# Performance work log

Measured on AMD Instinct MI355X. Metric: run time of the kernel, lower is better.

Reference implementation:

```python
import jax, jax.numpy as jnp
import numpy as np

_EPS = 1e-5
RC = 5.0   # cutoff radius
L = 20     # number of radial basis functions
N = 10000  # nodes
E = 100000 # edges
F = 128    # in_feats


def _ssp(x):
    # ShiftedSoftplus: softplus(x) - log(2)
    return jax.nn.softplus(x) - jnp.log(2.0)


def _rbf(r):
    # DimeNet radial basis: sqrt(2/rc) * sin(n*pi*r/rc) / r, n = 1..L.  r: [E,1] -> [E,L]
    n = jnp.arange(1, L + 1, dtype=r.dtype)
    return jnp.sqrt(2.0 / RC) * jnp.sin(n * jnp.pi * r / RC) / r


def _fc(u):
    # cosine cutoff applied elementwise: 0.5*(cos(pi*u/rc)+1) for u < rc else 0
    return jnp.where(u < RC, 0.5 * (jnp.cos(jnp.pi * u / RC) + 1.0), 0.0)


def setup_inputs() -> dict:
    key = jax.random.key(0)
    ks = jax.random.split(key, 12)

    def nrm(k, shape, scale=1.0):
        return jax.random.normal(k, shape, dtype=jnp.float32) * scale

    return {
        "x": nrm(ks[0], (N, 3)) * 3.0,           # atomic positions
        "v": nrm(ks[1], (N, F, 3)),               # vector node features
        "s": nrm(ks[2], (N, F)),                  # scalar node features
        "ms1_w": nrm(ks[3], (F, F), F ** -0.5),
        "ms1_b": jnp.zeros((F,), jnp.float32),
        "ms2_w": nrm(ks[4], (3 * F, F), F ** -0.5),
        "ms2_b": jnp.zeros((3 * F,), jnp.float32),
        "mv_w": nrm(ks[5], (3 * F, L), L ** -0.5),
        "mv_b": jnp.zeros((3 * F,), jnp.float32),
        "us1_w": nrm(ks[6], (F, F), F ** -0.5),
        "us1_b": jnp.zeros((F,), jnp.float32),
        "us2_w": nrm(ks[7], (3 * F, F), F ** -0.5),
        "us2_b": jnp.zeros((3 * F,), jnp.float32),
        "src": jax.random.randint(ks[8], (E,), 0, N, dtype=jnp.int32),
        "dst": jax.random.randint(ks[9], (E,), 0, N, dtype=jnp.int32),
    }


def reference(x, v, s, ms1_w, ms1_b, ms2_w, ms2_b, mv_w, mv_b,
              us1_w, us1_b, us2_w, us2_b, src, dst):
    # ---------- pass 1: message1 + reduce1 (sum over incoming edges) ----------
    sj = s[src]                                   # [E,F]   src scalar features
    vj = v[src]                                   # [E,F,3] src vector features
    vec = x[src] - x[dst]                         # [E,3]   x_i - x_j (molecule branch)
    r = jnp.sqrt(jnp.sum(vec ** 2, axis=-1) + _EPS)[:, None]          # [E,1]
    phi = _ssp(sj @ ms1_w.T + ms1_b) @ ms2_w.T + ms2_b                 # [E,3F]
    w = _fc(_rbf(r) @ mv_w.T + mv_b)                                    # [E,3F]
    v_, s_, r_ = jnp.split(phi * w, 3, axis=-1)                         # each [E,F]
    dv_e = vj * v_[:, :, None] + r_[:, :, None] * (vec / r)[:, None, :] # [E,F,3]
    dv = jax.ops.segment_sum(dv_e, dst, num_segments=N)                 # [N,F,3]
    ds = jax.ops.segment_sum(s_, dst, num_segments=N)                   # [N,F]
    v_new = v + dv
    s_new = s + ds

    # ---------- pass 2: message2 + reduce2 (mean over incoming edges) ----------
    s2 = _ssp(s_new[src] @ us1_w.T + us1_b) @ us2_w.T + us2_b           # [E,3F]
    deg = jax.ops.segment_sum(jnp.ones((E,), s.dtype), dst, num_segments=N)
    denom = jnp.maximum(deg, 1.0)
    s_mean = jax.ops.segment_sum(s2, dst, num_segments=N) / denom[:, None]        # [N,3F]
    uv = jax.ops.segment_sum(v_new[src], dst, num_segments=N) / denom[:, None, None]  # [N,F,3]
    avv, asv, ass = jnp.split(s_mean, 3, axis=-1)                       # each [N,F]
    norm = jnp.sqrt(jnp.sum(uv ** 2, axis=-1) + _EPS)[..., None]        # [N,F,1]
    dv2 = uv * avv[:, :, None]                                           # [N,F,3]
    ds2 = jnp.sum((uv / norm) ** 2, axis=-1) * asv + ass                 # [N,F]
    return (v_new + dv2, s_new + ds2)
```

## Files before the change

kernel.cpp:

```cpp
#include <hip/hip_runtime.h>
#include <hip/hip_bf16.h>


#define F_DIM   128
#define F3_DIM  384
#define L_DIM   20
#define CAP     64
#define BATCH   16

typedef __attribute__((ext_vector_type(8))) short short8;
typedef __attribute__((ext_vector_type(4))) float f32x4;
typedef __attribute__((ext_vector_type(4))) unsigned short us4;

struct u3 { unsigned a, b, c; };

__device__ __forceinline__ unsigned short f2bf(float f) {
  union { float f; unsigned u; } a; a.f = f;
  unsigned u = a.u;
  u = (u + 0x7FFFu + ((u >> 16) & 1u)) >> 16;
  return (unsigned short)u;
}
__device__ __forceinline__ float bf2f(unsigned short u) {
  union { unsigned u; float f; } a; a.u = ((unsigned)u) << 16;
  return a.f;
}

__global__ __launch_bounds__(256) void cast_fill_kernel(
    const float* __restrict__ ms1_w, unsigned short* __restrict__ w_ms1,
    const float* __restrict__ ms2_w, unsigned short* __restrict__ w_ms2,
    const float* __restrict__ us1_w, unsigned short* __restrict__ w_us1,
    const float* __restrict__ us2_w, unsigned short* __restrict__ w_us2,
    const float* __restrict__ s,     unsigned short* __restrict__ sbf,
    const float* __restrict__ v,     us4* __restrict__ v4,
    const float* __restrict__ mv_w,  unsigned short* __restrict__ mvwB,
    const int* __restrict__ src, const int* __restrict__ dst,
    int* __restrict__ cursor, int* __restrict__ jbuf,
    unsigned short* __restrict__ c1pad, unsigned short* __restrict__ v4pad,
    int nF, int E)
{
  int i = blockIdx.x * 256 + threadIdx.x;
  if (i < 16384) w_ms1[i] = f2bf(ms1_w[i]);
  if (i < 49152) w_ms2[i] = f2bf(ms2_w[i]);
  if (i < 16384) w_us1[i] = f2bf(us1_w[i]);
  if (i < 49152) w_us2[i] = f2bf(us2_w[i]);
  if (i < nF)    sbf[i] = f2bf(s[i]);
  if (i < nF) {
    const float* vp = v + (size_t)i * 3;
    us4 o; o.x = f2bf(vp[0]); o.y = f2bf(vp[1]); o.z = f2bf(vp[2]); o.w = 0;
    v4[i] = o;
  }
  if (i < 384 * 32) {
    int o = i >> 5, k = i & 31;
    float val = (k < 20) ? mv_w[o * 20 + k] * 0.6324555320336759f : 0.f;
    mvwB[i] = f2bf(val);
  }
  if (i < 768) c1pad[i] = 0;
  if (i < 512) v4pad[i] = 0;
  if (i < E) {
    int d = dst[i];
    int p = atomicAdd(&cursor[d], 1);
    if (p < CAP) jbuf[d * CAP + p] = src[i];
  }
}

__global__ __launch_bounds__(512) void mlp_kernel(
    const unsigned short* __restrict__ X,
    const unsigned short* __restrict__ W1,
    const float* __restrict__ B1,
    const unsigned short* __restrict__ W2,
    const float* __restrict__ B2,
    const us4* __restrict__ Vin,
    unsigned short* __restrict__ Yc)
{
  __shared__ float HT[128 * 17];
  const int lane = threadIdx.x & 63;
  const int wave = threadIdx.x >> 6;
  const int c    = lane & 15;
  const int quad = lane >> 4;
  const int m0   = blockIdx.x * 16;

  f32x4 acc = (f32x4){0.f, 0.f, 0.f, 0.f};
#pragma unroll
  for (int kk = 0; kk < 4; kk++) {
    short8 a = *(const short8*)(X + (size_t)(m0 + c) * 128 + kk * 32 + quad * 8);
    short8 b = *(const short8*)(W1 + (size_t)(wave * 16 + c) * 128 + kk * 32 + quad * 8);
    acc = __builtin_amdgcn_mfma_f32_16x16x32_bf16(a, b, acc, 0, 0, 0);
  }
  {
    int k = wave * 16 + c;
    float bias = B1[k];
#pragma unroll
    for (int r = 0; r < 4; r++) {
      float h = acc[r] + bias;
      float sp = (h > 15.f) ? h : log1pf(__expf(h));
      sp -= 0.69314718056f;
      HT[k * 17 + quad * 4 + r] = sp;
    }
  }
  __syncthreads();

  f32x4 acc2[3];
#pragma unroll
  for (int g = 0; g < 3; g++) acc2[g] = (f32x4){0.f, 0.f, 0.f, 0.f};
#pragma unroll
  for (int kk = 0; kk < 4; kk++) {
    short8 afr;
#pragma unroll
    for (int j = 0; j < 8; j++) {
      float hv = HT[(kk * 32 + quad * 8 + j) * 17 + c];
      afr[j] = (short)f2bf(hv);
    }
#pragma unroll
    for (int g = 0; g < 3; g++) {
      short8 b = *(const short8*)(W2 + (size_t)(g * 128 + wave * 16 + c) * 128 + kk * 32 + quad * 8);
      acc2[g] = __builtin_amdgcn_mfma_f32_16x16x32_bf16(afr, b, acc2[g], 0, 0, 0);
    }
  }
  {
    int f = wave * 16 + c;
    float b0 = B2[f], b1 = B2[128 + f], b2 = B2[256 + f];
#pragma unroll
    for (int r = 0; r < 4; r++) {
      int m = quad * 4 + r;
      us4 vv = Vin[(size_t)(m0 + m) * 128 + f];
      unsigned p0 = f2bf(acc2[0][r] + b0);
      unsigned p1 = f2bf(acc2[1][r] + b1);
      unsigned p2 = f2bf(acc2[2][r] + b2);
      u3 rec;
      rec.a = p0 | (p1 << 16);
      rec.b = p2 | ((unsigned)vv.x << 16);
      rec.c = (unsigned)vv.y | ((unsigned)vv.z << 16);
      *(u3*)(Yc + ((size_t)(m0 + m) * 128 + f) * 6) = rec;
    }
  }
}

__global__ __launch_bounds__(512) void hidden_kernel(
    const unsigned short* __restrict__ X,
    const unsigned short* __restrict__ W1,
    const float* __restrict__ B1,
    us4* __restrict__ V4)
{
  const int lane = threadIdx.x & 63;
  const int wave = threadIdx.x >> 6;
  const int c    = lane & 15;
  const int quad = lane >> 4;
  const int m0   = blockIdx.x * 16;

  f32x4 acc = (f32x4){0.f, 0.f, 0.f, 0.f};
#pragma unroll
  for (int kk = 0; kk < 4; kk++) {
    short8 a = *(const short8*)(X + (size_t)(m0 + c) * 128 + kk * 32 + quad * 8);
    short8 b = *(const short8*)(W1 + (size_t)(wave * 16 + c) * 128 + kk * 32 + quad * 8);
    acc = __builtin_amdgcn_mfma_f32_16x16x32_bf16(a, b, acc, 0, 0, 0);
  }
  int f = wave * 16 + c;
  float bias = B1[f];
#pragma unroll
  for (int r = 0; r < 4; r++) {
    int m = m0 + quad * 4 + r;
    float h = acc[r] + bias;
    float sp = (h > 15.f) ? h : log1pf(__expf(h));
    sp -= 0.69314718056f;
    unsigned short* wp = (unsigned short*)(V4 + (size_t)m * 128 + f) + 3;
    *wp = f2bf(sp);
  }
}

__global__ __launch_bounds__(256, 4) void pass1_kernel(
    const float* __restrict__ x,
    const unsigned short* __restrict__ combo1,
    const float* __restrict__ v,
    const float* __restrict__ s,
    const unsigned short* __restrict__ mvwB,
    const float* __restrict__ mv_b,
    const int* __restrict__ jbuf,
    const int* __restrict__ deg,
    float* __restrict__ vnew, us4* __restrict__ vnew4,
    float* __restrict__ snew, unsigned short* __restrict__ snew_bf, int nNodes)
{
  __shared__ unsigned short Asn[BATCH * 32];
  __shared__ float4 Au[BATCH];
  __shared__ us4 Wl[BATCH * 128];
  __shared__ float red[512];

  const int tid  = threadIdx.x;
  const int wave = tid >> 6, lane = tid & 63;
  const int half = wave >> 1, split = wave & 1;
  const int i = blockIdx.x;
  const int f = lane + 64 * half;
  const int c = lane & 15, quad = lane >> 4;

  int cnt = deg[i]; if (cnt > CAP) cnt = CAP;
  const int base = i * CAP;

  short8 bfr[6]; float bias[6];
#pragma unroll
  for (int p = 0; p < 3; p++)
#pragma unroll
    for (int h = 0; h < 2; h++) {
      int t = 2 * wave + h + 8 * p;
      bfr[p * 2 + h]  = *(const short8*)(mvwB + (size_t)(t * 16 + c) * 32 + quad * 8);
      bias[p * 2 + h] = mv_b[t * 16 + c];
    }

  const float xi0 = x[i * 3], xi1 = x[i * 3 + 1], xi2 = x[i * 3 + 2];
  int jv = (lane < cnt) ? jbuf[base + lane] : nNodes;

  float accV0 = 0.f, accV1 = 0.f, accV2 = 0.f, accS = 0.f;

  for (int bs = 0; bs < cnt; bs += BATCH) {
    int bcnt = cnt - bs; if (bcnt > BATCH) bcnt = BATCH;
    __syncthreads();

    if (wave == 0) {
      int t16 = lane & (BATCH - 1);
      int e = bs + t16;
      int j = __shfl(jv, e);
      if (lane < BATCH) {
        if (e < cnt) {
          float d0 = x[j * 3]     - xi0;
          float d1 = x[j * 3 + 1] - xi1;
          float d2 = x[j * 3 + 2] - xi2;
          float r = sqrtf(d0 * d0 + d1 * d1 + d2 * d2 + 1e-5f);
          float invr = 1.0f / r;
          Au[lane] = make_float4(d0 * invr, d1 * invr, d2 * invr, invr);
          float theta = r * 0.6283185307179586f;
          float s1, c1;
          __sincosf(theta, &s1, &c1);
          float c2 = 2.f * c1;
          float pm2 = s1, pm1 = c2 * s1;
          Asn[lane * 32 + 0] = f2bf(pm2);
          Asn[lane * 32 + 1] = f2bf(pm1);
#pragma unroll
          for (int l = 2; l < L_DIM; l++) {
            float cur = c2 * pm1 - pm2;
            Asn[lane * 32 + l] = f2bf(cur);
            pm2 = pm1; pm1 = cur;
          }
#pragma unroll
          for (int l = L_DIM; l < 32; l++) Asn[lane * 32 + l] = 0;
        } else {
          Au[lane] = make_float4(0.f, 0.f, 0.f, 0.f);
#pragma unroll
          for (int l = 0; l < 32; l++) Asn[lane * 32 + l] = 0;
        }
      }
    }
    __syncthreads();

    {
      short8 a = *(const short8*)&Asn[c * 32 + quad * 8];
      f32x4 acc[6];
#pragma unroll
      for (int q = 0; q < 6; q++)
        acc[q] = __builtin_amdgcn_mfma_f32_16x16x32_bf16(
            a, bfr[q], (f32x4){0.f, 0.f, 0.f, 0.f}, 0, 0, 0);
#pragma unroll
      for (int r = 0; r < 4; r++) {
        int el = quad * 4 + r;
        if (el < bcnt) {
          float invr = Au[el].w;
#pragma unroll
          for (int h = 0; h < 2; h++) {
            float wp0 = fmaf(acc[h][r],     invr, bias[h]);
            float wp1 = fmaf(acc[2 + h][r], invr, bias[2 + h]);
            float wp2 = fmaf(acc[4 + h][r], invr, bias[4 + h]);
            float w0 = (wp0 < 5.f) ? 0.5f * (__cosf(wp0 * 0.6283185307179586f) + 1.f) : 0.f;
            float w1 = (wp1 < 5.f) ? 0.5f * (__cosf(wp1 * 0.6283185307179586f) + 1.f) : 0.f;
            float w2 = (wp2 < 5.f) ? 0.5f * (__cosf(wp2 * 0.6283185307179586f) + 1.f) : 0.f;
            us4 o; o.x = f2bf(w0); o.y = f2bf(w1); o.z = f2bf(w2); o.w = 0;
            Wl[el * 128 + wave * 32 + h * 16 + c] = o;
          }
        } else {
          us4 z; z.x = 0; z.y = 0; z.z = 0; z.w = 0;
          Wl[el * 128 + wave * 32 + c]      = z;
          Wl[el * 128 + wave * 32 + 16 + c] = z;
        }
      }
    }
    __syncthreads();

    u3 cb[8];
#pragma unroll
    for (int k = 0; k < 8; k++) {
      int j = __shfl(jv, bs + split + 2 * k);
      cb[k] = *(const u3*)(combo1 + ((size_t)j * 128 + f) * 6);
    }
#pragma unroll
    for (int k = 0; k < 8; k++) {
      int el = split + 2 * k;
      float4 u = Au[el];
      us4 wv = Wl[el * 128 + f];
      float ph0 = bf2f((unsigned short)(cb[k].a & 0xffff));
      float ph1 = bf2f((unsigned short)(cb[k].a >> 16));
      float ph2 = bf2f((unsigned short)(cb[k].b & 0xffff));
      float vx  = bf2f((unsigned short)(cb[k].b >> 16));
      float vy  = bf2f((unsigned short)(cb[k].c & 0xffff));
      float vz  = bf2f((unsigned short)(cb[k].c >> 16));
      float m0 = ph0 * bf2f(wv.x);
      float m1 = ph1 * bf2f(wv.y);
      float m2 = ph2 * bf2f(wv.z);
      accV0 = fmaf(vx, m0, fmaf(m2, u.x, accV0));
      accV1 = fmaf(vy, m0, fmaf(m2, u.y, accV1));
      accV2 = fmaf(vz, m0, fmaf(m2, u.z, accV2));
      accS += m1;
    }
  }

  const int idx = half * 64 + lane;
  __syncthreads();
  if (split == 1) {
    red[idx * 4 + 0] = accV0; red[idx * 4 + 1] = accV1;
    red[idx * 4 + 2] = accV2; red[idx * 4 + 3] = accS;
  }
  __syncthreads();
  if (split == 0) {
    accV0 += red[idx * 4 + 0]; accV1 += red[idx * 4 + 1];
    accV2 += red[idx * 4 + 2]; accS  += red[idx * 4 + 3];
    size_t b3 = (size_t)i * 384 + f * 3;
    float n0 = v[b3] + accV0, n1 = v[b3 + 1] + accV1, n2 = v[b3 + 2] + accV2;
    vnew[b3] = n0; vnew[b3 + 1] = n1; vnew[b3 + 2] = n2;
    us4 o; o.x = f2bf(n0); o.y = f2bf(n1); o.z = f2bf(n2); o.w = 0;
    vnew4[(size_t)i * 128 + f] = o;
    size_t b1 = (size_t)i * 128 + f;
    float sv = s[b1] + accS;
    snew[b1] = sv;
    snew_bf[b1] = f2bf(sv);
  }
}

__global__ __launch_bounds__(256, 4) void pass2_kernel(
    const us4* __restrict__ vnew4,
    const int* __restrict__ jbuf, const int* __restrict__ deg,
    float* __restrict__ uvbuf,
    unsigned short* __restrict__ hmean,
    int nNodes)
{
  __shared__ float red[512];
  const int wave = threadIdx.x >> 6, lane = threadIdx.x & 63;
  const int half = wave >> 1, split = wave & 1;
  const int i = blockIdx.x;
  const int f = lane + 64 * half;

  int cnt = deg[i]; if (cnt > CAP) cnt = CAP;
  const int base = i * CAP;
  int jv = (lane < cnt) ? jbuf[base + lane] : nNodes;

  float accU0 = 0.f, accU1 = 0.f, accU2 = 0.f, accH = 0.f;

  for (int b0 = split; b0 < cnt; b0 += 16) {
    us4 cb[8];
#pragma unroll
    for (int k = 0; k < 8; k++) {
      int e = b0 + 2 * k;
      int ec = (e < 63) ? e : 63;
      int j = __shfl(jv, ec);
      cb[k] = vnew4[(size_t)j * 128 + f];
    }
#pragma unroll
    for (int k = 0; k < 8; k++) {
      accU0 += bf2f(cb[k].x);
      accU1 += bf2f(cb[k].y);
      accU2 += bf2f(cb[k].z);
      accH  += bf2f(cb[k].w);
    }
  }

  const int idx = half * 64 + lane;
  if (split == 1) {
    red[idx * 4 + 0] = accU0; red[idx * 4 + 1] = accU1;
    red[idx * 4 + 2] = accU2; red[idx * 4 + 3] = accH;
  }
  __syncthreads();
  if (split == 0) {
    accU0 += red[idx * 4 + 0]; accU1 += red[idx * 4 + 1];
    accU2 += red[idx * 4 + 2]; accH  += red[idx * 4 + 3];
    float dinv = 1.0f / (float)(cnt > 0 ? cnt : 1);
    size_t b3 = (size_t)i * 384 + f * 3;
    uvbuf[b3]     = accU0 * dinv;
    uvbuf[b3 + 1] = accU1 * dinv;
    uvbuf[b3 + 2] = accU2 * dinv;
    hmean[(size_t)i * 128 + f] = f2bf(accH * dinv);
  }
}

__global__ __launch_bounds__(512) void final_kernel(
    const unsigned short* __restrict__ Hm,
    const unsigned short* __restrict__ W2,
    const float* __restrict__ B2,
    const float* __restrict__ uvbuf,
    const float* __restrict__ vnew,
    const float* __restrict__ snew,
    const int* __restrict__ deg,
    float* __restrict__ vout, float* __restrict__ sout)
{
  const int lane = threadIdx.x & 63;
  const int wave = threadIdx.x >> 6;
  const int c    = lane & 15;
  const int quad = lane >> 4;
  const int m0   = blockIdx.x * 16;

  f32x4 acc2[3];
#pragma unroll
  for (int g = 0; g < 3; g++) acc2[g] = (f32x4){0.f, 0.f, 0.f, 0.f};
#pragma unroll
  for (int kk = 0; kk < 4; kk++) {
    short8 a = *(const short8*)(Hm + (size_t)(m0 + c) * 128 + kk * 32 + quad * 8);
#pragma unroll
    for (int g = 0; g < 3; g++) {
      short8 b = *(const short8*)(W2 + (size_t)(g * 128 + wave * 16 + c) * 128 + kk * 32 + quad * 8);
      acc2[g] = __builtin_amdgcn_mfma_f32_16x16x32_bf16(a, b, acc2[g], 0, 0, 0);
    }
  }

  int f = wave * 16 + c;
  float b0 = B2[f], b1 = B2[128 + f], b2 = B2[256 + f];
#pragma unroll
  for (int r = 0; r < 4; r++) {
    int m = m0 + quad * 4 + r;
    float z = (deg[m] > 0) ? 1.f : 0.f;
    float avv = (acc2[0][r] + b0) * z;
    float asv = (acc2[1][r] + b1) * z;
    float ass = (acc2[2][r] + b2) * z;
    size_t b3 = (size_t)m * 384 + f * 3;
    float uv0 = uvbuf[b3], uv1 = uvbuf[b3 + 1], uv2 = uvbuf[b3 + 2];
    float q = uv0 * uv0 + uv1 * uv1 + uv2 * uv2;
    float ds2 = (q / (q + 1e-5f)) * asv + ass;
    vout[b3]     = vnew[b3]     + uv0 * avv;
    vout[b3 + 1] = vnew[b3 + 1] + uv1 * avv;
    vout[b3 + 2] = vnew[b3 + 2] + uv2 * avv;
    size_t b1i = (size_t)m * 128 + f;
    sout[b1i] = snew[b1i] + ds2;
  }
}

extern "C" void kernel_launch(void* const* d_in, const int* in_sizes, int n_in,
                              void* d_out, int out_size, void* d_ws, size_t ws_size,
                              hipStream_t stream)
{
  const float* x     = (const float*)d_in[0];
  const float* v     = (const float*)d_in[1];
  const float* s     = (const float*)d_in[2];
  const float* ms1_w = (const float*)d_in[3];
  const float* ms1_b = (const float*)d_in[4];
  const float* ms2_w = (const float*)d_in[5];
  const float* ms2_b = (const float*)d_in[6];
  const float* mv_w  = (const float*)d_in[7];
  const float* mv_b  = (const float*)d_in[8];
  const float* us1_w = (const float*)d_in[9];
  const float* us1_b = (const float*)d_in[10];
  const float* us2_w = (const float*)d_in[11];
  const float* us2_b = (const float*)d_in[12];
  const int*   src   = (const int*)d_in[13];
  const int*   dst   = (const int*)d_in[14];

  const int N = in_sizes[0] / 3;
  const int E = in_sizes[13];

  char* p = (char*)d_ws;
  auto alloc = [&](size_t bytes) -> void* {
    void* r = (void*)p;
    p += (bytes + 255) & ~(size_t)255;
    return r;
  };
  unsigned short* sbf   = (unsigned short*)alloc((size_t)N * 128 * 2);
  unsigned short* snbf  = (unsigned short*)alloc((size_t)N * 128 * 2);
  unsigned short* w_ms1 = (unsigned short*)alloc(16384 * 2);
  unsigned short* w_ms2 = (unsigned short*)alloc(49152 * 2);
  unsigned short* w_us1 = (unsigned short*)alloc(16384 * 2);
  unsigned short* w_us2 = (unsigned short*)alloc(49152 * 2);
  unsigned short* mvwB  = (unsigned short*)alloc(384 * 32 * 2);
  us4*   v4     = (us4*)alloc((size_t)N * 128 * 8);
  us4*   vnew4  = (us4*)alloc((size_t)(N + 1) * 128 * 8);
  unsigned short* combo1 = (unsigned short*)alloc((size_t)(N + 1) * 128 * 12);
  float* uvbuf  = (float*)alloc((size_t)N * 384 * 4);
  unsigned short* hmean = (unsigned short*)alloc((size_t)N * 128 * 2);
  float* vnew   = (float*)alloc((size_t)N * 384 * 4);
  float* snew   = (float*)alloc((size_t)N * 128 * 4);
  int* cursor   = (int*)alloc((size_t)N * 4);
  int* jbuf     = (int*)alloc((size_t)N * CAP * 4);

  hipMemsetAsync(cursor, 0, (size_t)N * 4, stream);

  cast_fill_kernel<<<(N * 128 + 255) / 256, 256, 0, stream>>>(
      ms1_w, w_ms1, ms2_w, w_ms2, us1_w, w_us1, us2_w, w_us2,
      s, sbf, v, v4, mv_w, mvwB, src, dst, cursor, jbuf,
      combo1 + (size_t)N * 768, (unsigned short*)(vnew4 + (size_t)N * 128),
      N * 128, E);

  mlp_kernel<<<N / 16, 512, 0, stream>>>(sbf, w_ms1, ms1_b, w_ms2, ms2_b,
                                         v4, combo1);

  pass1_kernel<<<N, 256, 0, stream>>>(x, combo1, v, s, mvwB, mv_b,
                                      jbuf, cursor, vnew, vnew4, snew, snbf, N);

  hidden_kernel<<<N / 16, 512, 0, stream>>>(snbf, w_us1, us1_b, vnew4);

  pass2_kernel<<<N, 256, 0, stream>>>(vnew4, jbuf, cursor, uvbuf, hmean, N);

  float* vout = (float*)d_out;
  float* sout = vout + (size_t)N * 384;
  final_kernel<<<N / 16, 512, 0, stream>>>(hmean, w_us2, us2_b, uvbuf,
                                           vnew, snew, cursor, vout, sout);
}
```

Before: 226.0 us.

## Fuse pass2 gather-mean with final MLP and output kernel via shared memory

Merges the pass2 neighbor-mean kernel and the final projection kernel into one launch per 16-node tile. Each wave gathers two nodes' neighbor records and keeps the means and hidden vectors in shared memory, so the uvbuf/hmean round trip through global memory and one launch go away. It also drops the zero-fill of padded edge slots in pass1 in favour of bounds guards, and writes the hidden value as a full 8-byte record instead of a 2-byte store. The fused kernel walks edges serially per wave with fewer blocks, which may cut the latency hiding the gather gets.

```diff
diff --git a/kernel.cpp b/kernel.cpp
--- a/kernel.cpp
+++ b/kernel.cpp
@@ -162,8 +162,9 @@
     float h = acc[r] + bias;
     float sp = (h > 15.f) ? h : log1pf(__expf(h));
     sp -= 0.69314718056f;
-    unsigned short* wp = (unsigned short*)(V4 + (size_t)m * 128 + f) + 3;
-    *wp = f2bf(sp);
+    us4 rec = V4[(size_t)m * 128 + f];
+    rec.w = f2bf(sp);
+    V4[(size_t)m * 128 + f] = rec;
   }
 }
 
@@ -217,34 +218,28 @@
       int t16 = lane & (BATCH - 1);
       int e = bs + t16;
       int j = __shfl(jv, e);
-      if (lane < BATCH) {
-        if (e < cnt) {
-          float d0 = x[j * 3]     - xi0;
-          float d1 = x[j * 3 + 1] - xi1;
-          float d2 = x[j * 3 + 2] - xi2;
-          float r = sqrtf(d0 * d0 + d1 * d1 + d2 * d2 + 1e-5f);
-          float invr = 1.0f / r;
-          Au[lane] = make_float4(d0 * invr, d1 * invr, d2 * invr, invr);
-          float theta = r * 0.6283185307179586f;
-          float s1, c1;
-          __sincosf(theta, &s1, &c1);
-          float c2 = 2.f * c1;
-          float pm2 = s1, pm1 = c2 * s1;
-          Asn[lane * 32 + 0] = f2bf(pm2);
-          Asn[lane * 32 + 1] = f2bf(pm1);
-#pragma unroll
-          for (int l = 2; l < L_DIM; l++) {
-            float cur = c2 * pm1 - pm2;
-            Asn[lane * 32 + l] = f2bf(cur);
-            pm2 = pm1; pm1 = cur;
-          }
-#pragma unroll
-          for (int l = L_DIM; l < 32; l++) Asn[lane * 32 + l] = 0;
-        } else {
-          Au[lane] = make_float4(0.f, 0.f, 0.f, 0.f);
-#pragma unroll
-          for (int l = 0; l < 32; l++) Asn[lane * 32 + l] = 0;
+      if (lane < BATCH && e < cnt) {
+        float d0 = x[j * 3]     - xi0;
+        float d1 = x[j * 3 + 1] - xi1;
+        float d2 = x[j * 3 + 2] - xi2;
+        float r = sqrtf(d0 * d0 + d1 * d1 + d2 * d2 + 1e-5f);
+        float invr = 1.0f / r;
+        Au[lane] = make_float4(d0 * invr, d1 * invr, d2 * invr, invr);
+        float theta = r * 0.6283185307179586f;
+        float s1, c1;
+        __sincosf(theta, &s1, &c1);
+        float c2 = 2.f * c1;
+        float pm2 = s1, pm1 = c2 * s1;
+        Asn[lane * 32 + 0] = f2bf(pm2);
+        Asn[lane * 32 + 1] = f2bf(pm1);
+#pragma unroll
+        for (int l = 2; l < L_DIM; l++) {
+          float cur = c2 * pm1 - pm2;
+          Asn[lane * 32 + l] = f2bf(cur);
+          pm2 = pm1; pm1 = cur;
         }
+#pragma unroll
+        for (int l = L_DIM; l < 32; l++) Asn[lane * 32 + l] = 0;
       }
     }
     __syncthreads();
@@ -272,10 +267,6 @@
             us4 o; o.x = f2bf(w0); o.y = f2bf(w1); o.z = f2bf(w2); o.w = 0;
             Wl[el * 128 + wave * 32 + h * 16 + c] = o;
           }
-        } else {
-          us4 z; z.x = 0; z.y = 0; z.z = 0; z.w = 0;
-          Wl[el * 128 + wave * 32 + c]      = z;
-          Wl[el * 128 + wave * 32 + 16 + c] = z;
         }
       }
     }
@@ -290,21 +281,23 @@
 #pragma unroll
     for (int k = 0; k < 8; k++) {
       int el = split + 2 * k;
-      float4 u = Au[el];
-      us4 wv = Wl[el * 128 + f];
-      float ph0 = bf2f((unsigned short)(cb[k].a & 0xffff));
-      float ph1 = bf2f((unsigned short)(cb[k].a >> 16));
-      float ph2 = bf2f((unsigned short)(cb[k].b & 0xffff));
-      float vx  = bf2f((unsigned short)(cb[k].b >> 16));
-      float vy  = bf2f((unsigned short)(cb[k].c & 0xffff));
-      float vz  = bf2f((unsigned short)(cb[k].c >> 16));
-      float m0 = ph0 * bf2f(wv.x);
-      float m1 = ph1 * bf2f(wv.y);
-      float m2 = ph2 * bf2f(wv.z);
-      accV0 = fmaf(vx, m0, fmaf(m2, u.x, accV0));
-      accV1 = fmaf(vy, m0, fmaf(m2, u.y, accV1));
-      accV2 = fmaf(vz, m0, fmaf(m2, u.z, accV2));
-      accS += m1;
+      if (el < bcnt) {
+        float4 u = Au[el];
+        us4 wv = Wl[el * 128 + f];
+        float ph0 = bf2f((unsigned short)(cb[k].a & 0xffff));
+        float ph1 = bf2f((unsigned short)(cb[k].a >> 16));
+        float ph2 = bf2f((unsigned short)(cb[k].b & 0xffff));
+        float vx  = bf2f((unsigned short)(cb[k].b >> 16));
+        float vy  = bf2f((unsigned short)(cb[k].c & 0xffff));
+        float vz  = bf2f((unsigned short)(cb[k].c >> 16));
+        float m0 = ph0 * bf2f(wv.x);
+        float m1 = ph1 * bf2f(wv.y);
+        float m2 = ph2 * bf2f(wv.z);
+        accV0 = fmaf(vx, m0, fmaf(m2, u.x, accV0));
+        accV1 = fmaf(vy, m0, fmaf(m2, u.y, accV1));
+        accV2 = fmaf(vz, m0, fmaf(m2, u.z, accV2));
+        accS += m1;
+      }
     }
   }
 
@@ -330,107 +323,105 @@
   }
 }
 
-__global__ __launch_bounds__(256, 4) void pass2_kernel(
+__global__ __launch_bounds__(512, 2) void pass2_kernel(
     const us4* __restrict__ vnew4,
     const int* __restrict__ jbuf, const int* __restrict__ deg,
-    float* __restrict__ uvbuf,
-    unsigned short* __restrict__ hmean,
-    int nNodes)
-{
-  __shared__ float red[512];
-  const int wave = threadIdx.x >> 6, lane = threadIdx.x & 63;
-  const int half = wave >> 1, split = wave & 1;
-  const int i = blockIdx.x;
-  const int f = lane + 64 * half;
-
-  int cnt = deg[i]; if (cnt > CAP) cnt = CAP;
-  const int base = i * CAP;
-  int jv = (lane < cnt) ? jbuf[base + lane] : nNodes;
-
-  float accU0 = 0.f, accU1 = 0.f, accU2 = 0.f, accH = 0.f;
-
-  for (int b0 = split; b0 < cnt; b0 += 16) {
-    us4 cb[8];
-#pragma unroll
-    for (int k = 0; k < 8; k++) {
-      int e = b0 + 2 * k;
-      int ec = (e < 63) ? e : 63;
-      int j = __shfl(jv, ec);
-      cb[k] = vnew4[(size_t)j * 128 + f];
-    }
-#pragma unroll
-    for (int k = 0; k < 8; k++) {
-      accU0 += bf2f(cb[k].x);
-      accU1 += bf2f(cb[k].y);
-      accU2 += bf2f(cb[k].z);
-      accH  += bf2f(cb[k].w);
-    }
-  }
-
-  const int idx = half * 64 + lane;
-  if (split == 1) {
-    red[idx * 4 + 0] = accU0; red[idx * 4 + 1] = accU1;
-    red[idx * 4 + 2] = accU2; red[idx * 4 + 3] = accH;
-  }
-  __syncthreads();
-  if (split == 0) {
-    accU0 += red[idx * 4 + 0]; accU1 += red[idx * 4 + 1];
-    accU2 += red[idx * 4 + 2]; accH  += red[idx * 4 + 3];
-    float dinv = 1.0f / (float)(cnt > 0 ? cnt : 1);
-    size_t b3 = (size_t)i * 384 + f * 3;
-    uvbuf[b3]     = accU0 * dinv;
-    uvbuf[b3 + 1] = accU1 * dinv;
-    uvbuf[b3 + 2] = accU2 * dinv;
-    hmean[(size_t)i * 128 + f] = f2bf(accH * dinv);
-  }
-}
-
-__global__ __launch_bounds__(512) void final_kernel(
-    const unsigned short* __restrict__ Hm,
     const unsigned short* __restrict__ W2,
     const float* __restrict__ B2,
-    const float* __restrict__ uvbuf,
     const float* __restrict__ vnew,
     const float* __restrict__ snew,
-    const int* __restrict__ deg,
-    float* __restrict__ vout, float* __restrict__ sout)
-{
-  const int lane = threadIdx.x & 63;
-  const int wave = threadIdx.x >> 6;
-  const int c    = lane & 15;
-  const int quad = lane >> 4;
+    float* __restrict__ vout, float* __restrict__ sout, int nNodes)
+{
+  __shared__ unsigned short HMb[16][136];
+  __shared__ float UV[16 * 128 * 3];
+
+  const int tid  = threadIdx.x;
+  const int wave = tid >> 6, lane = tid & 63;
+  const int c    = lane & 15, quad = lane >> 4;
   const int m0   = blockIdx.x * 16;
 
+  const int ra = 2 * wave, rb = ra + 1;
+  const int na = m0 + ra, nb = m0 + rb;
+  int ca = deg[na]; if (ca > CAP) ca = CAP;
+  int cb = deg[nb]; if (cb > CAP) cb = CAP;
+  int jva = (lane < ca) ? jbuf[na * CAP + lane] : nNodes;
+  int jvb = (lane < cb) ? jbuf[nb * CAP + lane] : nNodes;
+
+  float a0l = 0.f, a1l = 0.f, a2l = 0.f, ahl = 0.f;
+  float a0h = 0.f, a1h = 0.f, a2h = 0.f, ahh = 0.f;
+  float b0l = 0.f, b1l = 0.f, b2l = 0.f, bhl = 0.f;
+  float b0h = 0.f, b1h = 0.f, b2h = 0.f, bhh = 0.f;
+
+  int emax = (ca > cb) ? ca : cb;
+  for (int e = 0; e < emax; ++e) {
+    int ja = __shfl(jva, e);
+    int jb = __shfl(jvb, e);
+    us4 ral = vnew4[(size_t)ja * 128 + lane];
+    us4 rah = vnew4[(size_t)ja * 128 + lane + 64];
+    us4 rbl = vnew4[(size_t)jb * 128 + lane];
+    us4 rbh = vnew4[(size_t)jb * 128 + lane + 64];
+    a0l += bf2f(ral.x); a1l += bf2f(ral.y); a2l += bf2f(ral.z); ahl += bf2f(ral.w);
+    a0h += bf2f(rah.x); a1h += bf2f(rah.y); a2h += bf2f(rah.z); ahh += bf2f(rah.w);
+    b0l += bf2f(rbl.x); b1l += bf2f(rbl.y); b2l += bf2f(rbl.z); bhl += bf2f(rbl.w);
+    b0h += bf2f(rbh.x); b1h += bf2f(rbh.y); b2h += bf2f(rbh.z); bhh += bf2f(rbh.w);
+  }
+
+  float dia = 1.0f / (float)(ca > 0 ? ca : 1);
+  float dib = 1.0f / (float)(cb > 0 ? cb : 1);
+  {
+    int fl = lane, fh = lane + 64;
+    UV[(ra * 128 + fl) * 3 + 0] = a0l * dia;
+    UV[(ra * 128 + fl) * 3 + 1] = a1l * dia;
+    UV[(ra * 128 + fl) * 3 + 2] = a2l * dia;
+    UV[(ra * 128 + fh) * 3 + 0] = a0h * dia;
+    UV[(ra * 128 + fh) * 3 + 1] = a1h * dia;
+    UV[(ra * 128 + fh) * 3 + 2] = a2h * dia;
+    UV[(rb * 128 + fl) * 3 + 0] = b0l * dib;
+    UV[(rb * 128 + fl) * 3 + 1] = b1l * dib;
+    UV[(rb * 128 + fl) * 3 + 2] = b2l * dib;
+    UV[(rb * 128 + fh) * 3 + 0] = b0h * dib;
+    UV[(rb * 128 + fh) * 3 + 1] = b1h * dib;
+    UV[(rb * 128 + fh) * 3 + 2] = b2h * dib;
+    HMb[ra][fl] = f2bf(ahl * dia);
+    HMb[ra][fh] = f2bf(ahh * dia);
+    HMb[rb][fl] = f2bf(bhl * dib);
+    HMb[rb][fh] = f2bf(bhh * dib);
+  }
+  __syncthreads();
+
   f32x4 acc2[3];
 #pragma unroll
   for (int g = 0; g < 3; g++) acc2[g] = (f32x4){0.f, 0.f, 0.f, 0.f};
 #pragma unroll
   for (int kk = 0; kk < 4; kk++) {
-    short8 a = *(const short8*)(Hm + (size_t)(m0 + c) * 128 + kk * 32 + quad * 8);
+    short8 afr = *(const short8*)&HMb[c][kk * 32 + quad * 8];
 #pragma unroll
     for (int g = 0; g < 3; g++) {
       short8 b = *(const short8*)(W2 + (size_t)(g * 128 + wave * 16 + c) * 128 + kk * 32 + quad * 8);
-      acc2[g] = __builtin_amdgcn_mfma_f32_16x16x32_bf16(a, b, acc2[g], 0, 0, 0);
+      acc2[g] = __builtin_amdgcn_mfma_f32_16x16x32_bf16(afr, b, acc2[g], 0, 0, 0);
     }
   }
 
   int f = wave * 16 + c;
-  float b0 = B2[f], b1 = B2[128 + f], b2 = B2[256 + f];
+  float bb0 = B2[f], bb1 = B2[128 + f], bb2 = B2[256 + f];
 #pragma unroll
   for (int r = 0; r < 4; r++) {
-    int m = m0 + quad * 4 + r;
-    float z = (deg[m] > 0) ? 1.f : 0.f;
-    float avv = (acc2[0][r] + b0) * z;
-    float asv = (acc2[1][r] + b1) * z;
-    float ass = (acc2[2][r] + b2) * z;
-    size_t b3 = (size_t)m * 384 + f * 3;
-    float uv0 = uvbuf[b3], uv1 = uvbuf[b3 + 1], uv2 = uvbuf[b3 + 2];
+    int m = quad * 4 + r;
+    int gm = m0 + m;
+    float z = (deg[gm] > 0) ? 1.f : 0.f;
+    float avv = (acc2[0][r] + bb0) * z;
+    float asv = (acc2[1][r] + bb1) * z;
+    float ass = (acc2[2][r] + bb2) * z;
+    float uv0 = UV[(m * 128 + f) * 3 + 0];
+    float uv1 = UV[(m * 128 + f) * 3 + 1];
+    float uv2 = UV[(m * 128 + f) * 3 + 2];
     float q = uv0 * uv0 + uv1 * uv1 + uv2 * uv2;
     float ds2 = (q / (q + 1e-5f)) * asv + ass;
+    size_t b3 = (size_t)gm * 384 + f * 3;
     vout[b3]     = vnew[b3]     + uv0 * avv;
     vout[b3 + 1] = vnew[b3 + 1] + uv1 * avv;
     vout[b3 + 2] = vnew[b3 + 2] + uv2 * avv;
-    size_t b1i = (size_t)m * 128 + f;
+    size_t b1i = (size_t)gm * 128 + f;
     sout[b1i] = snew[b1i] + ds2;
   }
 }
@@ -474,8 +465,6 @@
   us4*   v4     = (us4*)alloc((size_t)N * 128 * 8);
   us4*   vnew4  = (us4*)alloc((size_t)(N + 1) * 128 * 8);
   unsigned short* combo1 = (unsigned short*)alloc((size_t)(N + 1) * 128 * 12);
-  float* uvbuf  = (float*)alloc((size_t)N * 384 * 4);
-  unsigned short* hmean = (unsigned short*)alloc((size_t)N * 128 * 2);
   float* vnew   = (float*)alloc((size_t)N * 384 * 4);
   float* snew   = (float*)alloc((size_t)N * 128 * 4);
   int* cursor   = (int*)alloc((size_t)N * 4);
@@ -497,10 +486,8 @@
 
   hidden_kernel<<<N / 16, 512, 0, stream>>>(snbf, w_us1, us1_b, vnew4);
 
-  pass2_kernel<<<N, 256, 0, stream>>>(vnew4, jbuf, cursor, uvbuf, hmean, N);
-
   float* vout = (float*)d_out;
   float* sout = vout + (size_t)N * 384;
-  final_kernel<<<N / 16, 512, 0, stream>>>(hmean, w_us2, us2_b, uvbuf,
-                                           vnew, snew, cursor, vout, sout);
-}
+  pass2_kernel<<<N / 16, 512, 0, stream>>>(vnew4, jbuf, cursor, w_us2, us2_b,
+                                           vnew, snew, vout, sout, N);
+}
```

After: 213.3 us. 5.6% less time.
